# Kernel optimization log

Measured on AMD Instinct MI355X. Metric: run time of the kernel, lower is better.

## Reference

```python
import jax, jax.numpy as jnp
import numpy as np

N = 20000
E = 320000
H = 4
IN_DIM = 2000
# (in_dim, per-head out channels, concat) for each GATConv layer
LAYER_DIMS = [(2000, 128, True), (512, 64, True), (256, 32, True), (128, 64, False)]
NEG_SLOPE = 0.2  # PyG GATConv LeakyReLU slope


def setup_inputs() -> dict:
    key = jax.random.key(0)
    ks = jax.random.split(key, 2 + 4 * len(LAYER_DIMS))
    inp = {
        "x": jax.random.normal(ks[0], (N, IN_DIM), dtype=jnp.float32),
        "edge_index": jax.random.randint(ks[1], (2, E), 0, N, dtype=jnp.int64),
    }
    for i, (din, c, concat) in enumerate(LAYER_DIMS):
        k0, k1, k2, _ = jax.random.split(ks[2 + i], 4)
        inp[f"W{i}"] = (jax.random.normal(k0, (din, H * c), dtype=jnp.float32)
                         * (1.0 / np.sqrt(din)).astype(np.float32))
        inp[f"as{i}"] = jax.random.normal(k1, (H, c), dtype=jnp.float32) * 0.1
        inp[f"ad{i}"] = jax.random.normal(k2, (H, c), dtype=jnp.float32) * 0.1
        inp[f"b{i}"] = jnp.zeros((H * c if concat else c,), dtype=jnp.float32)
    return inp


def gat_conv(x, src, dst, W, att_src, att_dst, bias, concat):
    n, c = x.shape[0], W.shape[1] // H
    h = (x @ W).reshape(n, H, c)                      # (N,H,C) per-head features
    a_s = jnp.einsum("nhc,hc->nh", h, att_src)        # (N,H) source logits
    a_d = jnp.einsum("nhc,hc->nh", h, att_dst)        # (N,H) target logits
    e = a_s[src] + a_d[dst]                           # (E,H) per-edge logits
    e = jnp.where(e > 0, e, NEG_SLOPE * e)            # leaky_relu
    # segment softmax over edges sharing the same target node
    m = jax.ops.segment_max(e, dst, num_segments=n)   # (N,H)
    ex = jnp.exp(e - m[dst])
    denom = jax.ops.segment_sum(ex, dst, num_segments=n)
    alpha = ex / denom[dst]                           # (E,H)
    # weighted scatter-aggregate of source features
    out = jax.ops.segment_sum(alpha[:, :, None] * h[src], dst, num_segments=n)  # (N,H,C)
    out = out.reshape(n, H * c) if concat else out.mean(axis=1)
    return out + bias


def reference(x, edge_index, W0, as0, ad0, b0, W1, as1, ad1, b1,
              W2, as2, ad2, b2, W3, as3, ad3, b3):
    loops = jnp.arange(N, dtype=edge_index.dtype)
    src = jnp.concatenate([edge_index[0], loops])     # add self-loops (PyG default)
    dst = jnp.concatenate([edge_index[1], loops])
    params = [(W0, as0, ad0, b0), (W1, as1, ad1, b1), (W2, as2, ad2, b2), (W3, as3, ad3, b3)]
    h = x
    for i, (W, a_s, a_d, b) in enumerate(params):
        concat = LAYER_DIMS[i][2]
        h = gat_conv(h, src, dst, W, a_s, a_d, b, concat)
        if i < len(params) - 1:
            h = jax.nn.elu(h)  # dropout inactive in eval mode
    return h
```

## Files before the change

### kernel.cpp

```cpp
#include <hip/hip_runtime.h>
#include <hip/hip_bf16.h>

#define GN 20000
#define GE 320000
#define GETOT (GE + GN)
#define GH 4
#define NROW 20096

typedef __attribute__((ext_vector_type(8))) _Float16 f16x8;
typedef __attribute__((ext_vector_type(4))) float f32x4;

__global__ void detect_dtype_kernel(const void* __restrict__ ei, int* __restrict__ flag) {
    if (threadIdx.x == 0 && blockIdx.x == 0) {
        const long long* p = (const long long*)ei;
        int ok = 1;
        for (int i = 0; i < 16; ++i) {
            long long v = p[i];
            if (v < 0 || v >= GN) ok = 0;
        }
        *flag = ok;
    }
}

__device__ __forceinline__ int load_idx(const void* ei, int is64, long long pos) {
    if (is64) return (int)((const long long*)ei)[pos];
    return ((const int*)ei)[pos];
}

__global__ void hist_kernel(const void* __restrict__ ei, const int* __restrict__ flagp,
                            int* __restrict__ counts) {
    int e = blockIdx.x * blockDim.x + threadIdx.x;
    if (e >= GETOT) return;
    int d;
    if (e < GE) d = load_idx(ei, *flagp, (long long)GE + e);
    else        d = e - GE;
    atomicAdd(&counts[d], 1);
}

__global__ __launch_bounds__(1024) void scan_kernel(const int* __restrict__ counts,
                                                    int* __restrict__ offsets,
                                                    int* __restrict__ cursor) {
    __shared__ int sh[1024];
    const int tid = threadIdx.x;
    constexpr int CH = 20;
    const int base = tid * CH;
    int loc[CH];
    int sum = 0;
#pragma unroll
    for (int i = 0; i < CH; ++i) {
        int idx = base + i;
        int v = (idx < GN) ? counts[idx] : 0;
        loc[i] = sum;
        sum += v;
    }
    sh[tid] = sum;
    __syncthreads();
    for (int o = 1; o < 1024; o <<= 1) {
        int t = (tid >= o) ? sh[tid - o] : 0;
        __syncthreads();
        sh[tid] += t;
        __syncthreads();
    }
    const int excl = tid ? sh[tid - 1] : 0;
#pragma unroll
    for (int i = 0; i < CH; ++i) {
        int idx = base + i;
        if (idx < GN) {
            int o = excl + loc[i];
            offsets[idx] = o;
            cursor[idx]  = o;
        }
    }
    if (tid == 1023) offsets[GN] = sh[1023];
}

__global__ void scatter_kernel(const void* __restrict__ ei, const int* __restrict__ flagp,
                               int* __restrict__ cursor, int* __restrict__ csr_src) {
    int e = blockIdx.x * blockDim.x + threadIdx.x;
    if (e >= GETOT) return;
    int s, d;
    if (e < GE) {
        int is64 = *flagp;
        s = load_idx(ei, is64, e);
        d = load_idx(ei, is64, (long long)GE + e);
    } else {
        s = d = e - GE;
    }
    int pos = atomicAdd(&cursor[d], 1);
    csr_src[pos] = s;
}

__device__ __forceinline__ float h2f(unsigned u) {
    unsigned short us = (unsigned short)u;
    _Float16 h;
    __builtin_memcpy(&h, &us, 2);
    return (float)h;
}
__device__ __forceinline__ unsigned short f2h_bits(float v) {
    _Float16 h = (_Float16)v;
    unsigned short us;
    __builtin_memcpy(&us, &h, 2);
    return us;
}

__global__ void convert_wt(const float* __restrict__ W,
                           _Float16* __restrict__ thi,
                           int K, int N, int Kpad) {
    __shared__ float tile[32][33];
    int kb = blockIdx.x * 32, nb = blockIdx.y * 32;
    for (int i = threadIdx.y; i < 32; i += 8) {
        int k = kb + i, n = nb + threadIdx.x;
        tile[i][threadIdx.x] = (k < K) ? W[(size_t)k * N + n] : 0.f;
    }
    __syncthreads();
    for (int i = threadIdx.y; i < 32; i += 8) {
        int n = nb + i, k = kb + threadIdx.x;
        thi[(size_t)n * Kpad + k] = (_Float16)tile[threadIdx.x][i];
    }
}

__device__ __forceinline__ int swz(int a) { return a ^ (((a >> 6) & 7) << 4); }
__device__ __forceinline__ int invswz(int p) {
    int b8 = (p >> 8) & 1, b7 = (p >> 7) & 1;
    int a6 = ((p >> 6) & 1) ^ b8;
    int a5 = ((p >> 5) & 1) ^ b7;
    int a4 = ((p >> 4) & 1) ^ a6;
    return (p & ~0x70) | (a4 << 4) | (a5 << 5) | (a6 << 6);
}
__device__ __forceinline__ int swzA32(int a) { return a ^ (((a >> 7) & 7) << 4); }

#define GLDS16(gsrc, ldst) __builtin_amdgcn_global_load_lds( \
    (const __attribute__((address_space(1))) void*)(gsrc),   \
    (__attribute__((address_space(3))) void*)(ldst), 16, 0, 0)

template <int MODE>
__global__ __launch_bounds__(256, MODE == 1 ? 3 : 4) void gemm_f16(
        const void* __restrict__ Ap, int lda, int K,
        const _Float16* __restrict__ Whi,
        int Kpad, void* __restrict__ Cp, int M, int N, int NC) {
    constexpr int BUFB = (MODE == 1) ? 24576 : 16384;
    constexpr int WOFF = (MODE == 1) ? 16384 : 8192;
    __shared__ char lds[2 * BUFB];
    const int tid = threadIdx.x;

    const int nwg = gridDim.x;
    const int q = nwg >> 3, r = nwg & 7;
    const int xcd = blockIdx.x & 7, sub = blockIdx.x >> 3;
    const int orig = (xcd < r ? xcd * (q + 1) : r * (q + 1) + (xcd - r) * q) + sub;
    const int brow = (orig / NC) * 128;
    const int bcol = (orig % NC) * 128;

    const int lane = tid & 63, wid = tid >> 6;
    const int wr = wid >> 1, wc = wid & 1;
    const int l4 = lane & 15, kg = lane >> 4;

    int row8[2], ecol[2];
#pragma unroll
    for (int p = 0; p < 2; ++p) {
        int a = invswz(p * 4096 + tid * 16);
        row8[p] = a >> 6;
        ecol[p] = (a & 63) >> 1;
    }
    int rB[2];
#pragma unroll
    for (int p = 0; p < 2; ++p) rB[p] = bcol + row8[p];

    int rA2[2];
    int rA4[4], eA4[4];
    if constexpr (MODE == 1) {
#pragma unroll
        for (int p = 0; p < 4; ++p) {
            int a = swzA32(p * 4096 + tid * 16);
            int rr = brow + (a >> 7);
            rA4[p] = rr < M ? rr : M - 1;
            eA4[p] = (a & 127) >> 2;
        }
    } else {
#pragma unroll
        for (int p = 0; p < 2; ++p) rA2[p] = brow + row8[p];
    }
    const float*    A32 = (const float*)Ap;
    const _Float16* Af  = (const _Float16*)Ap;

    auto STAGE = [&](int buf, int k0) {
        char* bb = lds + buf * BUFB;
        if constexpr (MODE == 1) {
#pragma unroll
            for (int p = 0; p < 4; ++p) {
                int kk = k0 + eA4[p];
                if (kk >= K) kk = 0;
                GLDS16(A32 + (size_t)rA4[p] * lda + kk, bb + p * 4096 + tid * 16);
            }
        } else {
#pragma unroll
            for (int p = 0; p < 2; ++p)
                GLDS16(Af + (size_t)rA2[p] * lda + k0 + ecol[p], bb + p * 4096 + tid * 16);
        }
#pragma unroll
        for (int p = 0; p < 2; ++p)
            GLDS16(Whi + (size_t)rB[p] * Kpad + k0 + ecol[p], bb + WOFF + p * 4096 + tid * 16);
    };

    int aoff[4], boff[4];
#pragma unroll
    for (int m = 0; m < 4; ++m) {
        int row = wr * 64 + m * 16 + l4;
        aoff[m] = (MODE == 1) ? swzA32(row * 128 + kg * 32) : swz(row * 64 + kg * 16);
        boff[m] = swz((wc * 64 + m * 16 + l4) * 64 + kg * 16);
    }

    f32x4 acc[4][4];
#pragma unroll
    for (int m = 0; m < 4; ++m)
#pragma unroll
        for (int n = 0; n < 4; ++n) acc[m][n] = (f32x4)(0.f);

    const int nk = Kpad / 32;
    STAGE(0, 0);

    for (int t = 0; t < nk; ++t) {
        if (t + 1 < nk) {
            STAGE((t + 1) & 1, (t + 1) * 32);
            if constexpr (MODE == 1)
                asm volatile("s_waitcnt vmcnt(6)" ::: "memory");
            else
                asm volatile("s_waitcnt vmcnt(4)" ::: "memory");
        } else {
            asm volatile("s_waitcnt vmcnt(0)" ::: "memory");
        }
        __builtin_amdgcn_s_barrier();
        __builtin_amdgcn_sched_barrier(0);

        char* bb = lds + (t & 1) * BUFB;
        f16x8 av[4], wh[4];
        if constexpr (MODE == 1) {
            f32x4 u0[4], u1[4];
#pragma unroll
            for (int m = 0; m < 4; ++m) {
                u0[m] = *(const f32x4*)(bb + aoff[m]);
                u1[m] = *(const f32x4*)(bb + (aoff[m] ^ 16));
            }
            __builtin_amdgcn_sched_barrier(0);
#pragma unroll
            for (int n = 0; n < 4; ++n)
                wh[n] = *(const f16x8*)(bb + WOFF + boff[n]);
            __builtin_amdgcn_sched_barrier(0);
            asm volatile("s_waitcnt lgkmcnt(4)" ::: "memory");
            __builtin_amdgcn_sched_barrier(0);
#pragma unroll
            for (int m = 0; m < 4; ++m) {
                av[m][0] = (_Float16)u0[m].x; av[m][1] = (_Float16)u0[m].y;
                av[m][2] = (_Float16)u0[m].z; av[m][3] = (_Float16)u0[m].w;
                av[m][4] = (_Float16)u1[m].x; av[m][5] = (_Float16)u1[m].y;
                av[m][6] = (_Float16)u1[m].z; av[m][7] = (_Float16)u1[m].w;
            }
        } else {
#pragma unroll
            for (int m = 0; m < 4; ++m) av[m] = *(const f16x8*)(bb + aoff[m]);
#pragma unroll
            for (int n = 0; n < 4; ++n) wh[n] = *(const f16x8*)(bb + WOFF + boff[n]);
        }
        asm volatile("s_waitcnt lgkmcnt(0)" ::: "memory");
        __builtin_amdgcn_sched_barrier(0);

#pragma unroll
        for (int m = 0; m < 4; ++m)
#pragma unroll
            for (int n = 0; n < 4; ++n)
                acc[m][n] = __builtin_amdgcn_mfma_f32_16x16x32_f16(av[m], wh[n], acc[m][n], 0, 0, 0);
        __builtin_amdgcn_s_barrier();
    }

#pragma unroll
    for (int m = 0; m < 4; ++m) {
        int gr0 = brow + wr * 64 + m * 16 + (lane >> 4) * 4;
#pragma unroll
        for (int n = 0; n < 4; ++n) {
            int gc = bcol + wc * 64 + n * 16 + l4;
#pragma unroll
            for (int rr2 = 0; rr2 < 4; ++rr2) {
                int gr = gr0 + rr2;
                if (gr < M) {
                    size_t o = (size_t)gr * N + gc;
                    float v = acc[m][n][rr2];
                    if constexpr (MODE == 2) ((float*)Cp)[o] = v;
                    else                     ((_Float16*)Cp)[o] = (_Float16)v;
                }
            }
        }
    }
}

template <bool F16>
__global__ void att_sd_kernel(const void* __restrict__ hfeat,
                              const float* __restrict__ att_s,
                              const float* __restrict__ att_d,
                              float* __restrict__ a_s, float* __restrict__ a_d,
                              int C) {
    int wid  = (blockIdx.x * blockDim.x + threadIdx.x) >> 6;
    int lane = threadIdx.x & 63;
    if (wid >= GN) return;
#pragma unroll
    for (int h = 0; h < GH; ++h) {
        float ss = 0.f, sd = 0.f;
        for (int cc = lane; cc < C; cc += 64) {
            size_t idx = (size_t)wid * GH * C + h * C + cc;
            float v = F16 ? h2f(((const unsigned short*)hfeat)[idx])
                          : ((const float*)hfeat)[idx];
            ss += v * att_s[h * C + cc];
            sd += v * att_d[h * C + cc];
        }
#pragma unroll
        for (int o = 32; o; o >>= 1) {
            ss += __shfl_xor(ss, o);
            sd += __shfl_xor(sd, o);
        }
        if (lane == 0) { a_s[wid * GH + h] = ss; a_d[wid * GH + h] = sd; }
    }
}

template <int C, int CPT, int BLOCK>
__global__ __launch_bounds__(BLOCK) void gat_aggregate_f16(
        const unsigned short* __restrict__ hfeat,
        const float* __restrict__ a_s,
        const float* __restrict__ a_d,
        const int* __restrict__ offsets,
        const int* __restrict__ csr_src,
        const float* __restrict__ bias,
        unsigned short* __restrict__ of16) {
    constexpr int HC = GH * C;
    static_assert(BLOCK * CPT == HC, "coverage");
    const int n     = blockIdx.x;
    const int tid   = threadIdx.x;
    const int start = offsets[n];
    const int end   = offsets[n + 1];

    __shared__ float s_m[GH];
    __shared__ float s_den[GH];
    __shared__ int   s_src[64];
    __shared__ float s_al[GH][68];

    const float4 ad4 = *(const float4*)(a_d + n * GH);
    const float adh[GH] = {ad4.x, ad4.y, ad4.z, ad4.w};

    if (tid < 64) {
        float lmax[GH], lsum[GH];
#pragma unroll
        for (int h = 0; h < GH; ++h) lmax[h] = -1e30f;
        for (int e = start + tid; e < end; e += 64) {
            int s = csr_src[e];
            float4 as4 = *(const float4*)(a_s + s * GH);
            float l[GH] = {as4.x + adh[0], as4.y + adh[1], as4.z + adh[2], as4.w + adh[3]};
#pragma unroll
            for (int h = 0; h < GH; ++h) {
                float ll = l[h] > 0.f ? l[h] : 0.2f * l[h];
                lmax[h] = fmaxf(lmax[h], ll);
            }
        }
#pragma unroll
        for (int h = 0; h < GH; ++h)
#pragma unroll
            for (int o = 32; o; o >>= 1) lmax[h] = fmaxf(lmax[h], __shfl_xor(lmax[h], o));
#pragma unroll
        for (int h = 0; h < GH; ++h) lsum[h] = 0.f;
        for (int e = start + tid; e < end; e += 64) {
            int s = csr_src[e];
            float4 as4 = *(const float4*)(a_s + s * GH);
            float l[GH] = {as4.x + adh[0], as4.y + adh[1], as4.z + adh[2], as4.w + adh[3]};
#pragma unroll
            for (int h = 0; h < GH; ++h) {
                float ll = l[h] > 0.f ? l[h] : 0.2f * l[h];
                lsum[h] += __expf(ll - lmax[h]);
            }
        }
#pragma unroll
        for (int h = 0; h < GH; ++h)
#pragma unroll
            for (int o = 32; o; o >>= 1) lsum[h] += __shfl_xor(lsum[h], o);
        if (tid == 0) {
#pragma unroll
            for (int h = 0; h < GH; ++h) { s_m[h] = lmax[h]; s_den[h] = lsum[h]; }
        }
    }
    __syncthreads();

    float mm[GH], inv[GH];
#pragma unroll
    for (int h = 0; h < GH; ++h) { mm[h] = s_m[h]; inv[h] = 1.0f / s_den[h]; }

    const int ch0 = tid * CPT;
    const int hd  = ch0 / C;
    float acc[CPT];
#pragma unroll
    for (int j = 0; j < CPT; ++j) acc[j] = 0.f;

    for (int e0 = start; e0 < end; e0 += 64) {
        __syncthreads();
        if (tid < 64) {
            bool vld = (e0 + tid) < end;
            int s = vld ? csr_src[e0 + tid] : n;
            s_src[tid] = s;
            float4 as4 = *(const float4*)(a_s + s * GH);
            float l[GH] = {as4.x + adh[0], as4.y + adh[1], as4.z + adh[2], as4.w + adh[3]};
#pragma unroll
            for (int h = 0; h < GH; ++h) {
                float ll = l[h] > 0.f ? l[h] : 0.2f * l[h];
                s_al[h][tid] = vld ? __expf(ll - mm[h]) * inv[h] : 0.f;
            }
        }
        __syncthreads();
        int cnt = end - e0; if (cnt > 64) cnt = 64;
        int cnt4 = (cnt + 3) & ~3;
        for (int i = 0; i < cnt4; i += 4) {
            int4   ss = *(const int4*)&s_src[i];
            float4 aa = *(const float4*)&s_al[hd][i];
            if constexpr (CPT == 4) {
                uint2 v0 = ((const uint2*)(hfeat + (size_t)ss.x * HC))[tid];
                uint2 v1 = ((const uint2*)(hfeat + (size_t)ss.y * HC))[tid];
                uint2 v2 = ((const uint2*)(hfeat + (size_t)ss.z * HC))[tid];
                uint2 v3 = ((const uint2*)(hfeat + (size_t)ss.w * HC))[tid];
                acc[0] = fmaf(aa.x, h2f(v0.x & 0xffff), acc[0]);
                acc[1] = fmaf(aa.x, h2f(v0.x >> 16),    acc[1]);
                acc[2] = fmaf(aa.x, h2f(v0.y & 0xffff), acc[2]);
                acc[3] = fmaf(aa.x, h2f(v0.y >> 16),    acc[3]);
                acc[0] = fmaf(aa.y, h2f(v1.x & 0xffff), acc[0]);
                acc[1] = fmaf(aa.y, h2f(v1.x >> 16),    acc[1]);
                acc[2] = fmaf(aa.y, h2f(v1.y & 0xffff), acc[2]);
                acc[3] = fmaf(aa.y, h2f(v1.y >> 16),    acc[3]);
                acc[0] = fmaf(aa.z, h2f(v2.x & 0xffff), acc[0]);
                acc[1] = fmaf(aa.z, h2f(v2.x >> 16),    acc[1]);
                acc[2] = fmaf(aa.z, h2f(v2.y & 0xffff), acc[2]);
                acc[3] = fmaf(aa.z, h2f(v2.y >> 16),    acc[3]);
                acc[0] = fmaf(aa.w, h2f(v3.x & 0xffff), acc[0]);
                acc[1] = fmaf(aa.w, h2f(v3.x >> 16),    acc[1]);
                acc[2] = fmaf(aa.w, h2f(v3.y & 0xffff), acc[2]);
                acc[3] = fmaf(aa.w, h2f(v3.y >> 16),    acc[3]);
            } else {
                unsigned v0 = ((const unsigned*)(hfeat + (size_t)ss.x * HC))[tid];
                unsigned v1 = ((const unsigned*)(hfeat + (size_t)ss.y * HC))[tid];
                unsigned v2 = ((const unsigned*)(hfeat + (size_t)ss.z * HC))[tid];
                unsigned v3 = ((const unsigned*)(hfeat + (size_t)ss.w * HC))[tid];
                acc[0] = fmaf(aa.x, h2f(v0 & 0xffff), acc[0]);
                acc[1] = fmaf(aa.x, h2f(v0 >> 16),    acc[1]);
                acc[0] = fmaf(aa.y, h2f(v1 & 0xffff), acc[0]);
                acc[1] = fmaf(aa.y, h2f(v1 >> 16),    acc[1]);
                acc[0] = fmaf(aa.z, h2f(v2 & 0xffff), acc[0]);
                acc[1] = fmaf(aa.z, h2f(v2 >> 16),    acc[1]);
                acc[0] = fmaf(aa.w, h2f(v3 & 0xffff), acc[0]);
                acc[1] = fmaf(aa.w, h2f(v3 >> 16),    acc[1]);
            }
        }
    }

    unsigned short hs[CPT];
#pragma unroll
    for (int j = 0; j < CPT; ++j) {
        float v = acc[j] + bias[ch0 + j];
        v = v > 0.f ? v : expm1f(v);
        hs[j] = f2h_bits(v);
    }
    unsigned short* op = of16 + (size_t)n * HC + ch0;
    if constexpr (CPT == 4) {
        uint2 hw = make_uint2((unsigned)hs[0] | ((unsigned)hs[1] << 16),
                              (unsigned)hs[2] | ((unsigned)hs[3] << 16));
        *(uint2*)op = hw;
    } else {
        *(unsigned*)op = (unsigned)hs[0] | ((unsigned)hs[1] << 16);
    }
}

__global__ __launch_bounds__(128) void gat_aggregate_final(
        const float* __restrict__ hfeat,
        const float* __restrict__ a_s,
        const float* __restrict__ a_d,
        const int* __restrict__ offsets,
        const int* __restrict__ csr_src,
        const float* __restrict__ bias,
        float* __restrict__ outf) {
    constexpr int C = 64, HC = GH * C;
    const int n     = blockIdx.x;
    const int tid   = threadIdx.x;
    const int start = offsets[n];
    const int end   = offsets[n + 1];

    __shared__ float s_m[GH];
    __shared__ float s_den[GH];
    __shared__ int   s_src[64];
    __shared__ float s_al[GH][68];
    __shared__ float sacc[256];

    const float4 ad4 = *(const float4*)(a_d + n * GH);
    const float adh[GH] = {ad4.x, ad4.y, ad4.z, ad4.w};

    if (tid < 64) {
        float lmax[GH], lsum[GH];
#pragma unroll
        for (int h = 0; h < GH; ++h) lmax[h] = -1e30f;
        for (int e = start + tid; e < end; e += 64) {
            int s = csr_src[e];
            float4 as4 = *(const float4*)(a_s + s * GH);
            float l[GH] = {as4.x + adh[0], as4.y + adh[1], as4.z + adh[2], as4.w + adh[3]};
#pragma unroll
            for (int h = 0; h < GH; ++h) {
                float ll = l[h] > 0.f ? l[h] : 0.2f * l[h];
                lmax[h] = fmaxf(lmax[h], ll);
            }
        }
#pragma unroll
        for (int h = 0; h < GH; ++h)
#pragma unroll
            for (int o = 32; o; o >>= 1) lmax[h] = fmaxf(lmax[h], __shfl_xor(lmax[h], o));
#pragma unroll
        for (int h = 0; h < GH; ++h) lsum[h] = 0.f;
        for (int e = start + tid; e < end; e += 64) {
            int s = csr_src[e];
            float4 as4 = *(const float4*)(a_s + s * GH);
            float l[GH] = {as4.x + adh[0], as4.y + adh[1], as4.z + adh[2], as4.w + adh[3]};
#pragma unroll
            for (int h = 0; h < GH; ++h) {
                float ll = l[h] > 0.f ? l[h] : 0.2f * l[h];
                lsum[h] += __expf(ll - lmax[h]);
            }
        }
#pragma unroll
        for (int h = 0; h < GH; ++h)
#pragma unroll
            for (int o = 32; o; o >>= 1) lsum[h] += __shfl_xor(lsum[h], o);
        if (tid == 0) {
#pragma unroll
            for (int h = 0; h < GH; ++h) { s_m[h] = lmax[h]; s_den[h] = lsum[h]; }
        }
    }
    __syncthreads();

    float mm[GH], inv[GH];
#pragma unroll
    for (int h = 0; h < GH; ++h) { mm[h] = s_m[h]; inv[h] = 1.0f / s_den[h]; }

    const int hd = (2 * tid) / C;
    float2 acc = make_float2(0.f, 0.f);

    for (int e0 = start; e0 < end; e0 += 64) {
        __syncthreads();
        if (tid < 64) {
            bool vld = (e0 + tid) < end;
            int s = vld ? csr_src[e0 + tid] : n;
            s_src[tid] = s;
            float4 as4 = *(const float4*)(a_s + s * GH);
            float l[GH] = {as4.x + adh[0], as4.y + adh[1], as4.z + adh[2], as4.w + adh[3]};
#pragma unroll
            for (int h = 0; h < GH; ++h) {
                float ll = l[h] > 0.f ? l[h] : 0.2f * l[h];
                s_al[h][tid] = vld ? __expf(ll - mm[h]) * inv[h] : 0.f;
            }
        }
        __syncthreads();
        int cnt = end - e0; if (cnt > 64) cnt = 64;
        int cnt4 = (cnt + 3) & ~3;
        for (int i = 0; i < cnt4; i += 4) {
            int4   ss = *(const int4*)&s_src[i];
            float4 aa = *(const float4*)&s_al[hd][i];
            float2 v0 = ((const float2*)(hfeat + (size_t)ss.x * HC))[tid];
            float2 v1 = ((const float2*)(hfeat + (size_t)ss.y * HC))[tid];
            float2 v2 = ((const float2*)(hfeat + (size_t)ss.z * HC))[tid];
            float2 v3 = ((const float2*)(hfeat + (size_t)ss.w * HC))[tid];
            acc.x = fmaf(aa.x, v0.x, acc.x); acc.y = fmaf(aa.x, v0.y, acc.y);
            acc.x = fmaf(aa.y, v1.x, acc.x); acc.y = fmaf(aa.y, v1.y, acc.y);
            acc.x = fmaf(aa.z, v2.x, acc.x); acc.y = fmaf(aa.z, v2.y, acc.y);
            acc.x = fmaf(aa.w, v3.x, acc.x); acc.y = fmaf(aa.w, v3.y, acc.y);
        }
    }

    sacc[2 * tid]     = acc.x;
    sacc[2 * tid + 1] = acc.y;
    __syncthreads();
    if (tid < C) {
        float v = 0.f;
#pragma unroll
        for (int h = 0; h < GH; ++h) v += sacc[h * C + tid];
        outf[(size_t)n * C + tid] = v * (1.0f / GH) + bias[tid];
    }
}

extern "C" void kernel_launch(void* const* d_in, const int* in_sizes, int n_in,
                              void* d_out, int out_size, void* d_ws, size_t ws_size,
                              hipStream_t stream) {
    const float* x  = (const float*)d_in[0];
    const void*  ei = d_in[1];
    const float* W[4]  = {(const float*)d_in[2],  (const float*)d_in[6],
                          (const float*)d_in[10], (const float*)d_in[14]};
    const float* AS[4] = {(const float*)d_in[3],  (const float*)d_in[7],
                          (const float*)d_in[11], (const float*)d_in[15]};
    const float* AD[4] = {(const float*)d_in[4],  (const float*)d_in[8],
                          (const float*)d_in[12], (const float*)d_in[16]};
    const float* BI[4] = {(const float*)d_in[5],  (const float*)d_in[9],
                          (const float*)d_in[13], (const float*)d_in[17]};

    char*  w   = (char*)d_ws;
    size_t off = 0;
    auto alloc = [&](size_t b) -> char* {
        char* p = w + off;
        off += (b + 255) & ~(size_t)255;
        return p;
    };
    int*   flag    = (int*)alloc(4);
    int*   counts  = (int*)alloc((GN + 1) * sizeof(int));
    int*   offsets = (int*)alloc((GN + 1) * sizeof(int));
    int*   cursor  = (int*)alloc(GN * sizeof(int));
    int*   csr_src = (int*)alloc((size_t)GETOT * sizeof(int));
    float* a_s     = (float*)alloc((size_t)GN * GH * sizeof(float));
    float* a_d     = (float*)alloc((size_t)GN * GH * sizeof(float));
    unsigned short* hA = (unsigned short*)alloc((size_t)NROW * 512 * 2);
    unsigned short* hB = (unsigned short*)alloc((size_t)NROW * 512 * 2);
    float* hbuf    = (float*)alloc((size_t)NROW * 256 * sizeof(float));
    _Float16* wt   = (_Float16*)alloc((size_t)512 * 2016 * 2);
    (void)in_sizes; (void)n_in; (void)out_size; (void)ws_size;

    detect_dtype_kernel<<<1, 64, 0, stream>>>(ei, flag);
    hipMemsetAsync(counts, 0, (GN + 1) * sizeof(int), stream);
    int eblocks = (GETOT + 255) / 256;
    hist_kernel<<<eblocks, 256, 0, stream>>>(ei, flag, counts);
    scan_kernel<<<1, 1024, 0, stream>>>(counts, offsets, cursor);
    scatter_kernel<<<eblocks, 256, 0, stream>>>(ei, flag, cursor, csr_src);

    const dim3 tb(32, 8);
    const int NR = (GN + 127) / 128;

    convert_wt<<<dim3(2016 / 32, 512 / 32), tb, 0, stream>>>(W[0], wt, 2000, 512, 2016);
    gemm_f16<1><<<NR * 4, 256, 0, stream>>>(x, 2000, 2000, wt, 2016, hA, GN, 512, 4);
    att_sd_kernel<true><<<(GN * 64) / 256, 256, 0, stream>>>(hA, AS[0], AD[0], a_s, a_d, 128);
    gat_aggregate_f16<128, 4, 128><<<GN, 128, 0, stream>>>(hA, a_s, a_d, offsets, csr_src,
                                                           BI[0], hB);
    convert_wt<<<dim3(512 / 32, 256 / 32), tb, 0, stream>>>(W[1], wt, 512, 256, 512);
    gemm_f16<0><<<NR * 2, 256, 0, stream>>>(hB, 512, 512, wt, 512, hA, GN, 256, 2);
    att_sd_kernel<true><<<(GN * 64) / 256, 256, 0, stream>>>(hA, AS[1], AD[1], a_s, a_d, 64);
    gat_aggregate_f16<64, 4, 64><<<GN, 64, 0, stream>>>(hA, a_s, a_d, offsets, csr_src,
                                                        BI[1], hB);
    convert_wt<<<dim3(256 / 32, 128 / 32), tb, 0, stream>>>(W[2], wt, 256, 128, 256);
    gemm_f16<0><<<NR * 1, 256, 0, stream>>>(hB, 256, 256, wt, 256, hA, GN, 128, 1);
    att_sd_kernel<true><<<(GN * 64) / 256, 256, 0, stream>>>(hA, AS[2], AD[2], a_s, a_d, 32);
    gat_aggregate_f16<32, 2, 64><<<GN, 64, 0, stream>>>(hA, a_s, a_d, offsets, csr_src,
                                                        BI[2], hB);
    convert_wt<<<dim3(128 / 32, 256 / 32), tb, 0, stream>>>(W[3], wt, 128, 256, 128);
    gemm_f16<2><<<NR * 2, 256, 0, stream>>>(hB, 128, 128, wt, 128, hbuf, GN, 256, 2);
    att_sd_kernel<false><<<(GN * 64) / 256, 256, 0, stream>>>(hbuf, AS[3], AD[3], a_s, a_d, 64);
    gat_aggregate_final<<<GN, 128, 0, stream>>>(hbuf, a_s, a_d, offsets, csr_src,
                                                BI[3], (float*)d_out);
}
```

Before: 407.3 us.

## Fuse attention logit computation into GEMM epilogue with atomic accumulation

```diff
diff --git a/kernel.cpp b/kernel.cpp
--- a/kernel.cpp
+++ b/kernel.cpp
@@ -133,11 +133,13 @@
     (const __attribute__((address_space(1))) void*)(gsrc),   \
     (__attribute__((address_space(3))) void*)(ldst), 16, 0, 0)
 
-template <int MODE>
+template <int MODE, int CD>
 __global__ __launch_bounds__(256, MODE == 1 ? 3 : 4) void gemm_f16(
         const void* __restrict__ Ap, int lda, int K,
         const _Float16* __restrict__ Whi,
-        int Kpad, void* __restrict__ Cp, int M, int N, int NC) {
+        int Kpad, void* __restrict__ Cp, int M, int N, int NC,
+        const float* __restrict__ att_s, const float* __restrict__ att_d,
+        float* __restrict__ a_s, float* __restrict__ a_d) {
     constexpr int BUFB = (MODE == 1) ? 24576 : 16384;
     constexpr int WOFF = (MODE == 1) ? 16384 : 8192;
     __shared__ char lds[2 * BUFB];
@@ -271,51 +273,59 @@
         __builtin_amdgcn_s_barrier();
     }
 
+    float atS[4], atD[4];
+    int   hn[4];
+#pragma unroll
+    for (int n = 0; n < 4; ++n) {
+        int gc = bcol + wc * 64 + n * 16 + l4;
+        int hd = gc / CD;
+        hn[n]  = hd;
+        atS[n] = att_s[hd * CD + (gc - hd * CD)];
+        atD[n] = att_d[hd * CD + (gc - hd * CD)];
+    }
+
 #pragma unroll
     for (int m = 0; m < 4; ++m) {
         int gr0 = brow + wr * 64 + m * 16 + (lane >> 4) * 4;
 #pragma unroll
-        for (int n = 0; n < 4; ++n) {
-            int gc = bcol + wc * 64 + n * 16 + l4;
-#pragma unroll
-            for (int rr2 = 0; rr2 < 4; ++rr2) {
-                int gr = gr0 + rr2;
-                if (gr < M) {
-                    size_t o = (size_t)gr * N + gc;
-                    float v = acc[m][n][rr2];
-                    if constexpr (MODE == 2) ((float*)Cp)[o] = v;
-                    else                     ((_Float16*)Cp)[o] = (_Float16)v;
+        for (int rr2 = 0; rr2 < 4; ++rr2) {
+            int gr = gr0 + rr2;
+            float v0 = acc[m][0][rr2], v1 = acc[m][1][rr2];
+            float v2 = acc[m][2][rr2], v3 = acc[m][3][rr2];
+            if (gr < M) {
+                size_t ob = (size_t)gr * N + bcol + wc * 64 + l4;
+                if constexpr (MODE == 2) {
+                    float* C32 = (float*)Cp;
+                    C32[ob] = v0; C32[ob + 16] = v1; C32[ob + 32] = v2; C32[ob + 48] = v3;
+                } else {
+                    _Float16* C16 = (_Float16*)Cp;
+                    C16[ob] = (_Float16)v0; C16[ob + 16] = (_Float16)v1;
+                    C16[ob + 32] = (_Float16)v2; C16[ob + 48] = (_Float16)v3;
                 }
             }
-        }
-    }
-}
-
-template <bool F16>
-__global__ void att_sd_kernel(const void* __restrict__ hfeat,
-                              const float* __restrict__ att_s,
-                              const float* __restrict__ att_d,
-                              float* __restrict__ a_s, float* __restrict__ a_d,
-                              int C) {
-    int wid  = (blockIdx.x * blockDim.x + threadIdx.x) >> 6;
-    int lane = threadIdx.x & 63;
-    if (wid >= GN) return;
-#pragma unroll
-    for (int h = 0; h < GH; ++h) {
-        float ss = 0.f, sd = 0.f;
-        for (int cc = lane; cc < C; cc += 64) {
-            size_t idx = (size_t)wid * GH * C + h * C + cc;
-            float v = F16 ? h2f(((const unsigned short*)hfeat)[idx])
-                          : ((const float*)hfeat)[idx];
-            ss += v * att_s[h * C + cc];
-            sd += v * att_d[h * C + cc];
-        }
-#pragma unroll
-        for (int o = 32; o; o >>= 1) {
-            ss += __shfl_xor(ss, o);
-            sd += __shfl_xor(sd, o);
-        }
-        if (lane == 0) { a_s[wid * GH + h] = ss; a_d[wid * GH + h] = sd; }
+            float ps0 = v0 * atS[0] + v1 * atS[1];
+            float ps1 = v2 * atS[2] + v3 * atS[3];
+            float pd0 = v0 * atD[0] + v1 * atD[1];
+            float pd1 = v2 * atD[2] + v3 * atD[3];
+#pragma unroll
+            for (int o2 = 1; o2 < 16; o2 <<= 1) {
+                ps0 += __shfl_xor(ps0, o2);
+                ps1 += __shfl_xor(ps1, o2);
+                pd0 += __shfl_xor(pd0, o2);
+                pd1 += __shfl_xor(pd1, o2);
+            }
+            if (l4 == 0 && gr < M) {
+                if (hn[0] == hn[2]) {
+                    atomicAdd(&a_s[gr * GH + hn[0]], ps0 + ps1);
+                    atomicAdd(&a_d[gr * GH + hn[0]], pd0 + pd1);
+                } else {
+                    atomicAdd(&a_s[gr * GH + hn[0]], ps0);
+                    atomicAdd(&a_s[gr * GH + hn[2]], ps1);
+                    atomicAdd(&a_d[gr * GH + hn[0]], pd0);
+                    atomicAdd(&a_d[gr * GH + hn[2]], pd1);
+                }
+            }
+        }
     }
 }
 
@@ -608,8 +618,12 @@
     int*   offsets = (int*)alloc((GN + 1) * sizeof(int));
     int*   cursor  = (int*)alloc(GN * sizeof(int));
     int*   csr_src = (int*)alloc((size_t)GETOT * sizeof(int));
-    float* a_s     = (float*)alloc((size_t)GN * GH * sizeof(float));
-    float* a_d     = (float*)alloc((size_t)GN * GH * sizeof(float));
+    float* attb    = (float*)alloc((size_t)8 * GN * GH * sizeof(float));
+    float* aS[4], *aD[4];
+    for (int i = 0; i < 4; ++i) {
+        aS[i] = attb + (size_t)(2 * i)     * GN * GH;
+        aD[i] = attb + (size_t)(2 * i + 1) * GN * GH;
+    }
     unsigned short* hA = (unsigned short*)alloc((size_t)NROW * 512 * 2);
     unsigned short* hB = (unsigned short*)alloc((size_t)NROW * 512 * 2);
     float* hbuf    = (float*)alloc((size_t)NROW * 256 * sizeof(float));
@@ -618,6 +632,7 @@
 
     detect_dtype_kernel<<<1, 64, 0, stream>>>(ei, flag);
     hipMemsetAsync(counts, 0, (GN + 1) * sizeof(int), stream);
+    hipMemsetAsync(attb, 0, (size_t)8 * GN * GH * sizeof(float), stream);
     int eblocks = (GETOT + 255) / 256;
     hist_kernel<<<eblocks, 256, 0, stream>>>(ei, flag, counts);
     scan_kernel<<<1, 1024, 0, stream>>>(counts, offsets, cursor);
@@ -627,23 +642,23 @@
     const int NR = (GN + 127) / 128;
 
     convert_wt<<<dim3(2016 / 32, 512 / 32), tb, 0, stream>>>(W[0], wt, 2000, 512, 2016);
-    gemm_f16<1><<<NR * 4, 256, 0, stream>>>(x, 2000, 2000, wt, 2016, hA, GN, 512, 4);
-    att_sd_kernel<true><<<(GN * 64) / 256, 256, 0, stream>>>(hA, AS[0], AD[0], a_s, a_d, 128);
-    gat_aggregate_f16<128, 4, 128><<<GN, 128, 0, stream>>>(hA, a_s, a_d, offsets, csr_src,
+    gemm_f16<1, 128><<<NR * 4, 256, 0, stream>>>(x, 2000, 2000, wt, 2016, hA, GN, 512, 4,
+                                                 AS[0], AD[0], aS[0], aD[0]);
+    gat_aggregate_f16<128, 4, 128><<<GN, 128, 0, stream>>>(hA, aS[0], aD[0], offsets, csr_src,
                                                            BI[0], hB);
     convert_wt<<<dim3(512 / 32, 256 / 32), tb, 0, stream>>>(W[1], wt, 512, 256, 512);
-    gemm_f16<0><<<NR * 2, 256, 0, stream>>>(hB, 512, 512, wt, 512, hA, GN, 256, 2);
-    att_sd_kernel<true><<<(GN * 64) / 256, 256, 0, stream>>>(hA, AS[1], AD[1], a_s, a_d, 64);
-    gat_aggregate_f16<64, 4, 64><<<GN, 64, 0, stream>>>(hA, a_s, a_d, offsets, csr_src,
+    gemm_f16<0, 64><<<NR * 2, 256, 0, stream>>>(hB, 512, 512, wt, 512, hA, GN, 256, 2,
+                                                AS[1], AD[1], aS[1], aD[1]);
+    gat_aggregate_f16<64, 4, 64><<<GN, 64, 0, stream>>>(hA, aS[1], aD[1], offsets, csr_src,
                                                         BI[1], hB);
     convert_wt<<<dim3(256 / 32, 128 / 32), tb, 0, stream>>>(W[2], wt, 256, 128, 256);
-    gemm_f16<0><<<NR * 1, 256, 0, stream>>>(hB, 256, 256, wt, 256, hA, GN, 128, 1);
-    att_sd_kernel<true><<<(GN * 64) / 256, 256, 0, stream>>>(hA, AS[2], AD[2], a_s, a_d, 32);
-    gat_aggregate_f16<32, 2, 64><<<GN, 64, 0, stream>>>(hA, a_s, a_d, offsets, csr_src,
+    gemm_f16<0, 32><<<NR * 1, 256, 0, stream>>>(hB, 256, 256, wt, 256, hA, GN, 128, 1,
+                                                AS[2], AD[2], aS[2], aD[2]);
+    gat_aggregate_f16<32, 2, 64><<<GN, 64, 0, stream>>>(hA, aS[2], aD[2], offsets, csr_src,
                                                         BI[2], hB);
     convert_wt<<<dim3(128 / 32, 256 / 32), tb, 0, stream>>>(W[3], wt, 128, 256, 128);
-    gemm_f16<2><<<NR * 2, 256, 0, stream>>>(hB, 128, 128, wt, 128, hbuf, GN, 256, 2);
-    att_sd_kernel<false><<<(GN * 64) / 256, 256, 0, stream>>>(hbuf, AS[3], AD[3], a_s, a_d, 64);
-    gat_aggregate_final<<<GN, 128, 0, stream>>>(hbuf, a_s, a_d, offsets, csr_src,
+    gemm_f16<2, 64><<<NR * 2, 256, 0, stream>>>(hB, 128, 128, wt, 128, hbuf, GN, 256, 2,
+                                                AS[3], AD[3], aS[3], aD[3]);
+    gat_aggregate_final<<<GN, 128, 0, stream>>>(hbuf, aS[3], aD[3], offsets, csr_src,
                                                 BI[3], (float*)d_out);
 }
```

Result: faster. 398.3 us (-2.2%).
